# Kernel optimization log

Hardware: AMD Instinct MI355X
Metric: run time of the kernel (lower is better)

Reference implementation:

```python
import math
import jax, jax.numpy as jnp
import numpy as np

B, S, HID = 2, 1024, 2048
H, D, R = 16, 128, 64            # heads, head_dim, rope_dim_per_head
KVC, QC = 512, 1536              # kv / query compressed dims
MAX_POS = 4096


def _lin(x, w, b):
    return x @ w.T + b


def _rotate_half(x):
    x1, x2 = x[..., : x.shape[-1] // 2], x[..., x.shape[-1] // 2 :]
    return jnp.concatenate([-x2, x1], axis=-1)


def _rope_tables(dim, end, theta=10000.0):
    freqs = 1.0 / (theta ** (jnp.arange(0, dim, 2)[: dim // 2].astype(jnp.float32) / dim))
    f = jnp.outer(jnp.arange(end, dtype=jnp.float32), freqs)  # [end, dim//2]
    cos, sin = jnp.cos(f), jnp.sin(f)
    # duplicate halves so tables broadcast against the full rope dim (standard HF convention)
    return jnp.concatenate([cos, cos], -1), jnp.concatenate([sin, sin], -1)


def setup_inputs() -> dict:
    key = jax.random.key(0)
    ks = jax.random.split(key, 17)
    w = lambda k, shape: (jax.random.normal(k, shape, jnp.float32) * 0.02)
    return {
        "hidden_states": jax.random.normal(ks[0], (B, S, HID), jnp.float32),
        "W_DKV_w": w(ks[1], (KVC, HID)),  "W_DKV_b": w(ks[2], (KVC,)),
        "W_UK_w":  w(ks[3], (H * D, KVC)), "W_UK_b":  w(ks[4], (H * D,)),
        "W_UV_w":  w(ks[5], (H * D, KVC)), "W_UV_b":  w(ks[6], (H * D,)),
        "W_KR_w":  w(ks[7], (R, D)),       "W_KR_b":  w(ks[8], (R,)),
        "W_DQ_w":  w(ks[9], (QC, HID)),    "W_DQ_b":  w(ks[10], (QC,)),
        "W_UQ_w":  w(ks[11], (H * D, QC)), "W_UQ_b":  w(ks[12], (H * D,)),
        "W_QR_w":  w(ks[13], (R, D)),      "W_QR_b":  w(ks[14], (R,)),
        "W_O_w":   w(ks[15], (HID, H * D)),"W_O_b":   w(ks[16], (HID,)),
    }


def reference(hidden_states, W_DKV_w, W_DKV_b, W_UK_w, W_UK_b, W_UV_w, W_UV_b,
              W_KR_w, W_KR_b, W_DQ_w, W_DQ_b, W_UQ_w, W_UQ_b,
              W_QR_w, W_QR_b, W_O_w, W_O_b):
    b, s = hidden_states.shape[:2]
    # latent KV compression + decompression
    c_kv = _lin(hidden_states, W_DKV_w, W_DKV_b)                      # [B,S,KVC]
    k = _lin(c_kv, W_UK_w, W_UK_b).reshape(b, s, H, D)
    v = _lin(c_kv, W_UV_w, W_UV_b).reshape(b, s, H, D)
    # latent Q compression + decompression
    c_q = _lin(hidden_states, W_DQ_w, W_DQ_b)                         # [B,S,QC]
    q = _lin(c_q, W_UQ_w, W_UQ_b).reshape(b, s, H, D)
    # decoupled rope sub-dims
    k_r = _lin(k, W_KR_w, W_KR_b)                                     # [B,S,H,R]
    q_r = _lin(q, W_QR_w, W_QR_b)                                     # [B,S,H,R]
    cos, sin = _rope_tables(R, MAX_POS)
    cos_p = cos[:s][:, None, :]                                       # [S,1,R] -> broadcast over B,H
    sin_p = sin[:s][:, None, :]
    q_r = q_r * cos_p + _rotate_half(q_r) * sin_p
    k_r = k_r * cos_p + _rotate_half(k_r) * sin_p
    # SDPA (no mask, no causal flag in original)
    scale = 1.0 / math.sqrt(D)
    scores = jnp.einsum("bqhd,bkhd->bhqk", q, k) * scale              # [B,H,S,S]
    probs = jax.nn.softmax(scores, axis=-1)
    attn = jnp.einsum("bhqk,bkhd->bqhd", probs, v).reshape(b, s, H * D)
    output = _lin(attn, W_O_w, W_O_b)                                 # [B,S,HID]
    return output, c_kv, k_r
```

## Files before the change

kernel.cpp:

```cpp
#include <hip/hip_runtime.h>
#include <cstdint>

typedef __bf16 bf16;
typedef __attribute__((ext_vector_type(8))) __bf16 bf16x8;
typedef __attribute__((ext_vector_type(4))) float f32x4;

#define MFMA16(a, b, c) __builtin_amdgcn_mfma_f32_16x16x32_bf16(a, b, c, 0, 0, 0)

__device__ __forceinline__ void async16(const bf16* g, bf16* l) {
  __builtin_amdgcn_global_load_lds(
      (const __attribute__((address_space(1))) void*)g,
      (__attribute__((address_space(3))) void*)l, 16, 0, 0);
}

__device__ __forceinline__ bf16x8 load8cvt(const float* p) {
  f32x4 a = *(const f32x4*)p;
  f32x4 b = *(const f32x4*)(p + 4);
  bf16x8 r;
  r[0] = (bf16)a[0]; r[1] = (bf16)a[1]; r[2] = (bf16)a[2]; r[3] = (bf16)a[3];
  r[4] = (bf16)b[0]; r[5] = (bf16)b[1]; r[6] = (bf16)b[2]; r[7] = (bf16)b[3];
  return r;
}

__global__ __launch_bounds__(256) void cvt_f32_bf16(const float* __restrict__ src,
                                                    bf16* __restrict__ dst, int n) {
  int i = (blockIdx.x * 256 + threadIdx.x) * 8;
  if (i >= n) return;
  *(bf16x8*)(dst + i) = load8cvt(src + i);
}

__global__ __launch_bounds__(256) void cvt6(
    const float* __restrict__ s0, bf16* __restrict__ d0, int n0,
    const float* __restrict__ s1, bf16* __restrict__ d1, int n1,
    const float* __restrict__ s2, bf16* __restrict__ d2, int n2,
    const float* __restrict__ s3, bf16* __restrict__ d3, int n3,
    const float* __restrict__ s4, bf16* __restrict__ d4, int n4,
    const float* __restrict__ s5, bf16* __restrict__ d5, int n5) {
  const float* s; bf16* d; int n;
  switch (blockIdx.y) {
    case 0: s = s0; d = d0; n = n0; break;
    case 1: s = s1; d = d1; n = n1; break;
    case 2: s = s2; d = d2; n = n2; break;
    case 3: s = s3; d = d3; n = n3; break;
    case 4: s = s4; d = d4; n = n4; break;
    default: s = s5; d = d5; n = n5; break;
  }
  int i = (blockIdx.x * 256 + threadIdx.x) * 8;
  if (i >= n) return;
  *(bf16x8*)(d + i) = load8cvt(s + i);
}

template <int MODE>
__global__ __launch_bounds__(256) void gemm_bb(
    const bf16* __restrict__ A, int lda,
    const bf16* __restrict__ Bm, int ldb,
    const float* __restrict__ bias0, const float* __restrict__ bias1, int nsplit,
    bf16* __restrict__ outb, float* __restrict__ outf, int ldo,
    int M, int N, int K) {
  __shared__ __align__(16) bf16 As[2][128 * 32];
  __shared__ __align__(16) bf16 Bs[2][64 * 32];
  const int t = threadIdx.x;
  const int lane = t & 63, w = t >> 6;
  const int quad = lane >> 4, l15 = lane & 15;

  const int nwg = gridDim.x * gridDim.y;
  const int id = blockIdx.y * gridDim.x + blockIdx.x;
  const int sw = (id & 7) * (nwg >> 3) + (id >> 3);
  const int bm = (sw / gridDim.x) * 128, bn = (sw % gridDim.x) * 64;

  const int wm = (w >> 1) * 64, wn = (w & 1) * 32;

  f32x4 acc[4][2] = {};

  const int srow = t >> 2;
  const int scol = (t & 3) * 8;
  const bf16* Ap = A + (int64_t)(bm + srow) * lda + scol;
  const bf16* Bp = Bm + (int64_t)(bn + srow) * ldb + scol;

  auto STAGE = [&](int buf, int k0) {
    async16(Ap + k0, &As[buf][w * 512]);
    async16(Ap + (int64_t)64 * lda + k0, &As[buf][2048 + w * 512]);
    async16(Bp + k0, &Bs[buf][w * 512]);
  };
  auto COMPUTE = [&](int buf) {
    bf16x8 a[4], bq[2];
#pragma unroll
    for (int mt = 0; mt < 4; ++mt)
      a[mt] = *(const bf16x8*)(&As[buf][(wm + mt * 16 + l15) * 32 + quad * 8]);
#pragma unroll
    for (int nt = 0; nt < 2; ++nt)
      bq[nt] = *(const bf16x8*)(&Bs[buf][(wn + nt * 16 + l15) * 32 + quad * 8]);
#pragma unroll
    for (int mt = 0; mt < 4; ++mt)
#pragma unroll
      for (int nt = 0; nt < 2; ++nt)
        acc[mt][nt] = MFMA16(a[mt], bq[nt], acc[mt][nt]);
  };

  STAGE(0, 0);
  for (int k0 = 0; k0 < K; k0 += 64) {
    STAGE(1, k0 + 32);
    asm volatile("s_waitcnt vmcnt(3)\n\ts_barrier" ::: "memory");
    COMPUTE(0);
    asm volatile("s_waitcnt lgkmcnt(0)\n\ts_barrier" ::: "memory");
    if (k0 + 64 < K) {
      STAGE(0, k0 + 64);
      asm volatile("s_waitcnt vmcnt(3)\n\ts_barrier" ::: "memory");
    } else {
      asm volatile("s_waitcnt vmcnt(0)\n\ts_barrier" ::: "memory");
    }
    COMPUTE(1);
    asm volatile("s_waitcnt lgkmcnt(0)\n\ts_barrier" ::: "memory");
  }

  float bv[2];
#pragma unroll
  for (int nt = 0; nt < 2; ++nt) {
    int n = bn + wn + nt * 16 + l15;
    bv[nt] = (n < nsplit) ? bias0[n] : bias1[n - nsplit];
  }
#pragma unroll
  for (int mt = 0; mt < 4; ++mt)
#pragma unroll
    for (int nt = 0; nt < 2; ++nt)
#pragma unroll
      for (int r = 0; r < 4; ++r) {
        int64_t m = bm + wm + mt * 16 + quad * 4 + r;
        int n = bn + wn + nt * 16 + l15;
        float v = acc[mt][nt][r] + bv[nt];
        if (MODE != 1) outb[m * ldo + n] = (bf16)v;
        if (MODE == 1) outf[m * (int64_t)ldo + n] = v;
        if (MODE == 2 && n < nsplit) outf[m * nsplit + n] = v;
      }
}

__global__ __launch_bounds__(256) void kr_rope(const bf16* __restrict__ kmat,
                                               const float* __restrict__ Wkr,
                                               const float* __restrict__ bkr,
                                               float* __restrict__ krout) {
  const int t = threadIdx.x;
  const int lane = t & 63, w = t >> 6;
  const int quad = lane >> 4, l15 = lane & 15;
  const int row0 = blockIdx.x * 64 + w * 16;

  const int rr = row0 + l15;
  const bf16* krow = kmat + (int64_t)(rr >> 4) * 4096 + (rr & 15) * 128;
  bf16x8 af[4];
#pragma unroll
  for (int ks = 0; ks < 4; ++ks)
    af[ks] = *(const bf16x8*)(krow + ks * 32 + quad * 8);

  f32x4 acc[4] = {};
#pragma unroll
  for (int nt = 0; nt < 4; ++nt)
#pragma unroll
    for (int ks = 0; ks < 4; ++ks) {
      bf16x8 bf_ = load8cvt(Wkr + (nt * 16 + l15) * 128 + ks * 32 + quad * 8);
      acc[nt] = MFMA16(af[ks], bf_, acc[nt]);
    }

  float bv[4], fr[4];
#pragma unroll
  for (int nt = 0; nt < 4; ++nt) {
    bv[nt] = bkr[nt * 16 + l15];
    int j = ((nt & 1) * 16 + l15);
    fr[nt] = exp2f(-(float)j * 0.41524101186092034f);
  }

#pragma unroll
  for (int r = 0; r < 4; ++r) {
    int row = row0 + quad * 4 + r;
    int pos = (row >> 4) & 1023;
    float val[4];
#pragma unroll
    for (int nt = 0; nt < 4; ++nt) val[nt] = acc[nt][r] + bv[nt];
#pragma unroll
    for (int nt = 0; nt < 4; ++nt) {
      int n = nt * 16 + l15;
      float ang = (float)pos * fr[nt];
      float c = cosf(ang), s = sinf(ang);
      float partner = val[nt ^ 2];
      float o = val[nt] * c + ((nt < 2) ? -partner : partner) * s;
      krout[(int64_t)row * 64 + n] = o;
    }
  }
}

__global__ __launch_bounds__(256) void attn_fwd(const bf16* __restrict__ q,
                                                const bf16* __restrict__ k,
                                                const bf16* __restrict__ v,
                                                bf16* __restrict__ attn) {
  const int qt = blockIdx.x, bh = blockIdx.y;
  const int b = bh >> 4, h = bh & 15;
  __shared__ __align__(16) bf16 Kt[64 * 136];
  __shared__ __align__(16) bf16 Vt[128 * 72];
  __shared__ __align__(16) bf16 Pl[4][16 * 72];

  const int t = threadIdx.x;
  const int lane = t & 63, w = t >> 6;
  const int quad = lane >> 4, l15 = lane & 15;
  const int trow = b * 1024 + qt * 64 + w * 16;
  const float scale = 0.08838834764831845f;

  bf16x8 qf[4];
#pragma unroll
  for (int ks = 0; ks < 4; ++ks)
    qf[ks] = *(const bf16x8*)(q + (int64_t)(trow + l15) * 2048 + h * 128 +
                              ks * 32 + quad * 8);

  const int skey = t >> 4;
  const int sd0 = (t & 15) * 8;
  const bf16* kp = k + (int64_t)b * 1024 * 4096 + h * 128 + sd0;
  const bf16* vp = v + (int64_t)b * 1024 * 4096 + h * 128 + sd0;

  bf16x8 kreg[4], vreg[4];
#pragma unroll
  for (int r = 0; r < 4; ++r) {
    kreg[r] = *(const bf16x8*)(kp + (int64_t)(r * 16 + skey) * 4096);
    vreg[r] = *(const bf16x8*)(vp + (int64_t)(r * 16 + skey) * 4096);
  }

  f32x4 o[8] = {};
  float lrow[4] = {0.f, 0.f, 0.f, 0.f};

  for (int kt = 0; kt < 16; ++kt) {
#pragma unroll
    for (int r = 0; r < 4; ++r) {
      int key = r * 16 + skey;
      *(bf16x8*)(Kt + key * 136 + sd0) = kreg[r];
      int col = (((key >> 3) ^ ((sd0 >> 3) & 7)) << 3) + (key & 7);
#pragma unroll
      for (int j = 0; j < 8; ++j) Vt[(sd0 + j) * 72 + col] = vreg[r][j];
    }
    __syncthreads();

    if (kt + 1 < 16) {
      const bf16* kn = kp + (int64_t)(kt + 1) * 64 * 4096;
      const bf16* vn = vp + (int64_t)(kt + 1) * 64 * 4096;
#pragma unroll
      for (int r = 0; r < 4; ++r) {
        kreg[r] = *(const bf16x8*)(kn + (int64_t)(r * 16 + skey) * 4096);
        vreg[r] = *(const bf16x8*)(vn + (int64_t)(r * 16 + skey) * 4096);
      }
    }

    f32x4 s[4] = {};
    __builtin_amdgcn_s_setprio(1);
#pragma unroll
    for (int nt = 0; nt < 4; ++nt)
#pragma unroll
      for (int ks = 0; ks < 4; ++ks) {
        bf16x8 bfrg = *(const bf16x8*)(Kt + (nt * 16 + l15) * 136 + ks * 32 + quad * 8);
        s[nt] = MFMA16(qf[ks], bfrg, s[nt]);
      }
    __builtin_amdgcn_s_setprio(0);

    float rsum[4] = {0.f, 0.f, 0.f, 0.f};
#pragma unroll
    for (int nt = 0; nt < 4; ++nt)
#pragma unroll
      for (int r = 0; r < 4; ++r) {
        float p = __expf(s[nt][r] * scale);
        rsum[r] += p;
        int row = quad * 4 + r;
        int blk = (nt * 2 + (l15 >> 3)) ^ (quad * 2 + (r >> 1));
        Pl[w][row * 72 + (blk << 3) + (l15 & 7)] = (bf16)p;
      }
#pragma unroll
    for (int r = 0; r < 4; ++r) lrow[r] += rsum[r];

    __builtin_amdgcn_s_setprio(1);
#pragma unroll
    for (int ks = 0; ks < 2; ++ks) {
      int ablk = (ks * 4 + quad) ^ (l15 >> 1);
      bf16x8 afrg = *(const bf16x8*)(&Pl[w][l15 * 72 + (ablk << 3)]);
#pragma unroll
      for (int dt = 0; dt < 8; ++dt) {
        int d = dt * 16 + l15;
        int kb = ((ks * 4 + quad) ^ ((d >> 3) & 7)) << 3;
        bf16x8 bfrg = *(const bf16x8*)(Vt + d * 72 + kb);
        o[dt] = MFMA16(afrg, bfrg, o[dt]);
      }
    }
    __builtin_amdgcn_s_setprio(0);
    __syncthreads();
  }

  float inv[4];
#pragma unroll
  for (int r = 0; r < 4; ++r) {
    float ssum = lrow[r];
#pragma unroll
    for (int off = 8; off >= 1; off >>= 1) ssum += __shfl_xor(ssum, off, 64);
    inv[r] = 1.0f / ssum;
  }
#pragma unroll
  for (int dt = 0; dt < 8; ++dt)
#pragma unroll
    for (int r = 0; r < 4; ++r) {
      int64_t row = trow + quad * 4 + r;
      int col = h * 128 + dt * 16 + l15;
      attn[row * 2048 + col] = (bf16)(o[dt][r] * inv[r]);
    }
}

extern "C" void kernel_launch(void* const* d_in, const int* in_sizes, int n_in,
                              void* d_out, int out_size, void* d_ws, size_t ws_size,
                              hipStream_t stream) {
  const float* hidden = (const float*)d_in[0];
  const float* Wdkv = (const float*)d_in[1];
  const float* bdkv = (const float*)d_in[2];
  const float* Wuk  = (const float*)d_in[3];
  const float* buk  = (const float*)d_in[4];
  const float* Wuv  = (const float*)d_in[5];
  const float* buv  = (const float*)d_in[6];
  const float* Wkr  = (const float*)d_in[7];
  const float* bkr  = (const float*)d_in[8];
  const float* Wdq  = (const float*)d_in[9];
  const float* bdq  = (const float*)d_in[10];
  const float* Wuq  = (const float*)d_in[11];
  const float* buq  = (const float*)d_in[12];
  const float* Wo   = (const float*)d_in[15];
  const float* bo   = (const float*)d_in[16];

  float* out0 = (float*)d_out;
  float* c_kv = out0 + 4194304;
  float* k_r  = out0 + 5242880;

  bf16* DKVQ = (bf16*)d_ws;
  bf16* KV   = DKVQ + 4194304;

  bf16* WT   = KV;
  bf16* qx   = (bf16*)out0;
  bf16* hb   = qx + 4194304;
  bf16* WUKV = qx;
  bf16* Wuqb = hb;
  bf16* Wob  = (bf16*)k_r;

  cvt6<<<dim3(2048, 6), 256, 0, stream>>>(
      hidden, hb, 4194304,
      Wdkv, WT, 1048576,
      Wdq, WT + 1048576, 3145728,
      Wuk, WUKV, 1048576,
      Wuv, WUKV + 1048576, 1048576,
      Wo, Wob, 4194304);
  gemm_bb<2><<<dim3(32, 16), 256, 0, stream>>>(hb, 2048, WT, 2048, bdkv, bdq, 512,
                                               DKVQ, c_kv, 2048, 2048, 2048, 2048);
  cvt_f32_bf16<<<1536, 256, 0, stream>>>(Wuq, Wuqb, 3145728);
  gemm_bb<0><<<dim3(64, 16), 256, 0, stream>>>(DKVQ, 2048, WUKV, 512, buk, buv, 2048,
                                               KV, nullptr, 4096, 2048, 4096, 512);
  gemm_bb<0><<<dim3(32, 16), 256, 0, stream>>>(DKVQ + 512, 2048, Wuqb, 1536, buq, buq,
                                               2048, qx, nullptr, 2048, 2048, 2048, 1536);
  attn_fwd<<<dim3(16, 32), 256, 0, stream>>>(qx, KV, KV + 2048, DKVQ);
  gemm_bb<1><<<dim3(32, 16), 256, 0, stream>>>(DKVQ, 2048, Wob, 2048, bo, bo, 2048,
                                               nullptr, out0, 2048, 2048, 2048, 2048);
  kr_rope<<<512, 256, 0, stream>>>(KV, Wkr, bkr, k_r);
}
```

Baseline: 310.2 us.

## Widen attention blocks to 128 queries and load K fragments directly from global

The attention kernel now uses 512-thread blocks covering 128 query rows, with the grid remapped so the four heads of a group sit in adjacent blocks. K is no longer staged through shared memory: each wave loads its MFMA B-fragments straight from global into registers every key tile, which drops the K LDS buffer and its store traffic. Only V goes through LDS, with the staging split across twice as many threads. The cost is more redundant global and L2 reads of K (eight waves each fetch the full tile), unprefetched K loads sitting on the critical path, and higher register pressure from sixteen fragment registers under a 512x2 launch bound.

```diff
diff --git a/kernel.cpp b/kernel.cpp
--- a/kernel.cpp
+++ b/kernel.cpp
@@ -186,20 +186,20 @@
   }
 }
 
-__global__ __launch_bounds__(256) void attn_fwd(const bf16* __restrict__ q,
-                                                const bf16* __restrict__ k,
-                                                const bf16* __restrict__ v,
-                                                bf16* __restrict__ attn) {
-  const int qt = blockIdx.x, bh = blockIdx.y;
+__global__ __launch_bounds__(512, 2) void attn_fwd(const bf16* __restrict__ q,
+                                                   const bf16* __restrict__ k,
+                                                   const bf16* __restrict__ v,
+                                                   bf16* __restrict__ attn) {
+  const int bh = blockIdx.x * 4 + (blockIdx.y >> 3);
+  const int qt = blockIdx.y & 7;
   const int b = bh >> 4, h = bh & 15;
-  __shared__ __align__(16) bf16 Kt[64 * 136];
   __shared__ __align__(16) bf16 Vt[128 * 72];
-  __shared__ __align__(16) bf16 Pl[4][16 * 72];
+  __shared__ __align__(16) bf16 Pl[8][16 * 72];
 
   const int t = threadIdx.x;
   const int lane = t & 63, w = t >> 6;
   const int quad = lane >> 4, l15 = lane & 15;
-  const int trow = b * 1024 + qt * 64 + w * 16;
+  const int trow = b * 1024 + qt * 128 + w * 16;
   const float scale = 0.08838834764831845f;
 
   bf16x8 qf[4];
@@ -208,26 +208,24 @@
     qf[ks] = *(const bf16x8*)(q + (int64_t)(trow + l15) * 2048 + h * 128 +
                               ks * 32 + quad * 8);
 
+  const bf16* kbase = k + (int64_t)b * 1024 * 4096 + h * 128;
+
   const int skey = t >> 4;
   const int sd0 = (t & 15) * 8;
-  const bf16* kp = k + (int64_t)b * 1024 * 4096 + h * 128 + sd0;
   const bf16* vp = v + (int64_t)b * 1024 * 4096 + h * 128 + sd0;
 
-  bf16x8 kreg[4], vreg[4];
-#pragma unroll
-  for (int r = 0; r < 4; ++r) {
-    kreg[r] = *(const bf16x8*)(kp + (int64_t)(r * 16 + skey) * 4096);
-    vreg[r] = *(const bf16x8*)(vp + (int64_t)(r * 16 + skey) * 4096);
-  }
+  bf16x8 vreg[2];
+#pragma unroll
+  for (int r = 0; r < 2; ++r)
+    vreg[r] = *(const bf16x8*)(vp + (int64_t)(r * 32 + skey) * 4096);
 
   f32x4 o[8] = {};
   float lrow[4] = {0.f, 0.f, 0.f, 0.f};
 
   for (int kt = 0; kt < 16; ++kt) {
 #pragma unroll
-    for (int r = 0; r < 4; ++r) {
-      int key = r * 16 + skey;
-      *(bf16x8*)(Kt + key * 136 + sd0) = kreg[r];
+    for (int r = 0; r < 2; ++r) {
+      int key = r * 32 + skey;
       int col = (((key >> 3) ^ ((sd0 >> 3) & 7)) << 3) + (key & 7);
 #pragma unroll
       for (int j = 0; j < 8; ++j) Vt[(sd0 + j) * 72 + col] = vreg[r][j];
@@ -235,24 +233,26 @@
     __syncthreads();
 
     if (kt + 1 < 16) {
-      const bf16* kn = kp + (int64_t)(kt + 1) * 64 * 4096;
-      const bf16* vn = vp + (int64_t)(kt + 1) * 64 * 4096;
-#pragma unroll
-      for (int r = 0; r < 4; ++r) {
-        kreg[r] = *(const bf16x8*)(kn + (int64_t)(r * 16 + skey) * 4096);
-        vreg[r] = *(const bf16x8*)(vn + (int64_t)(r * 16 + skey) * 4096);
-      }
-    }
-
+#pragma unroll
+      for (int r = 0; r < 2; ++r)
+        vreg[r] = *(const bf16x8*)(vp + (int64_t)((kt + 1) * 64 + r * 32 + skey) * 4096);
+    }
+
+    const bf16* kp = kbase + (int64_t)kt * 64 * 4096;
+    bf16x8 kf[16];
+#pragma unroll
+    for (int nt = 0; nt < 4; ++nt)
+#pragma unroll
+      for (int ks = 0; ks < 4; ++ks)
+        kf[nt * 4 + ks] = *(const bf16x8*)(kp + (int64_t)(nt * 16 + l15) * 4096 +
+                                           ks * 32 + quad * 8);
     f32x4 s[4] = {};
     __builtin_amdgcn_s_setprio(1);
 #pragma unroll
     for (int nt = 0; nt < 4; ++nt)
 #pragma unroll
-      for (int ks = 0; ks < 4; ++ks) {
-        bf16x8 bfrg = *(const bf16x8*)(Kt + (nt * 16 + l15) * 136 + ks * 32 + quad * 8);
-        s[nt] = MFMA16(qf[ks], bfrg, s[nt]);
-      }
+      for (int ks = 0; ks < 4; ++ks)
+        s[nt] = MFMA16(qf[ks], kf[nt * 4 + ks], s[nt]);
     __builtin_amdgcn_s_setprio(0);
 
     float rsum[4] = {0.f, 0.f, 0.f, 0.f};
@@ -351,7 +351,7 @@
                                                KV, nullptr, 4096, 2048, 4096, 512);
   gemm_bb<0><<<dim3(32, 16), 256, 0, stream>>>(DKVQ + 512, 2048, Wuqb, 1536, buq, buq,
                                                2048, qx, nullptr, 2048, 2048, 2048, 1536);
-  attn_fwd<<<dim3(16, 32), 256, 0, stream>>>(qx, KV, KV + 2048, DKVQ);
+  attn_fwd<<<dim3(8, 32), 512, 0, stream>>>(qx, KV, KV + 2048, DKVQ);
   gemm_bb<1><<<dim3(32, 16), 256, 0, stream>>>(DKVQ, 2048, Wob, 2048, bo, bo, 2048,
                                                nullptr, out0, 2048, 2048, 2048, 2048);
   kr_rope<<<512, 256, 0, stream>>>(KV, Wkr, bkr, k_r);
```

After: 352.0 us. 1.13x slower.
